# Optimization experiments

Hardware: AMD Instinct MI355X
Metric: run time of the kernel (lower is better)

## Reference

```python
import jax, jax.numpy as jnp
import numpy as np

N, C, D = 131072, 512, 3


def setup_inputs() -> dict:
    key = jax.random.key(0)
    kx, kmu = jax.random.split(key)
    X = jax.random.normal(kx, (N, D), dtype=jnp.float32)
    mu = jax.random.normal(kmu, (C, D), dtype=jnp.float32)
    w = jnp.zeros((C,), dtype=jnp.float32)
    # sigma as in __init__: r = sqrt(sum of per-dim unbiased variances of mu0)
    r = jnp.sqrt(jnp.var(mu, axis=0, ddof=1).sum())
    sigma = (0.1 * (r / C ** (1.0 / D))).astype(jnp.float32)
    return {"X": X, "mu": mu, "w": w, "sigma": sigma}


def reference(X, mu, w, sigma):
    # One EM step of a uniform-covariance GMM (EM_step_pytorch).
    n, d = X.shape
    # pairwise squared distances [N, C]
    D2_nc = ((X[:, None, :] - mu[None, :, :]) ** 2).sum(-1)
    # log-responsibilities (E-step), softmax over components
    lgamma_nc = jax.nn.log_softmax(w[None, :] - D2_nc / (2.0 * sigma ** 2), axis=1)
    gamma_nc = jnp.exp(lgamma_nc)
    # M-step: centroids (softmax over points, per component)
    mu_new = jax.nn.softmax(lgamma_nc, axis=0).T @ X  # [C, D]
    # M-step: component scores
    h_c = jax.nn.logsumexp(lgamma_nc, axis=0)  # [C]
    w_new = h_c - h_c.mean()
    # M-step: uniform std
    sigma_new = jnp.sqrt((gamma_nc * D2_nc).sum() / (d * n))
    # EM values: expected targets and free energy
    Y = gamma_nc @ mu_new  # [N, D]
    logpi_c = w_new - jax.nn.logsumexp(w_new)
    Cfe = (gamma_nc * (
        ((mu_new ** 2).sum(-1)[None, :] - (Y ** 2).sum(-1)[:, None]) / (2.0 * sigma_new ** 2)
        + d * jnp.log(sigma_new)
        - logpi_c[None, :]
        + lgamma_nc
    )).sum()
    return Y, Cfe
```

## Files before the change

kernel.cpp:

```cpp
#include <hip/hip_runtime.h>
#include <cfloat>
#include <cmath>

#define NPTS 131072
#define NC   512
#define NREP 4

#define PM4_OFF  0
#define PQ4_OFF  2048
#define ST4_OFF  4096
#define MISC_OFF 12288

__device__ __forceinline__ float waveSum(float v) {
#pragma unroll
  for (int off = 32; off > 0; off >>= 1) v += __shfl_down(v, off, 64);
  return v;
}
__device__ __forceinline__ float waveMax(float v) {
#pragma unroll
  for (int off = 32; off > 0; off >>= 1) v = fmaxf(v, __shfl_down(v, off, 64));
  return v;
}

__global__ __launch_bounds__(512) void k_prep(
    const float* __restrict__ mu, const float* __restrict__ w,
    const float* __restrict__ sigma, float4* __restrict__ pm,
    float* __restrict__ ST, float* __restrict__ misc) {
  const int t = threadIdx.x;
  const float sg = sigma[0];
  const float inv2s2 = 1.0f / (2.0f * sg * sg);
  const float m0 = mu[3 * t], m1 = mu[3 * t + 1], m2 = mu[3 * t + 2];
  pm[t] = make_float4(2.0f * inv2s2 * m0, 2.0f * inv2s2 * m1, 2.0f * inv2s2 * m2,
                      w[t] - (m0 * m0 + m1 * m1 + m2 * m2) * inv2s2);
#pragma unroll
  for (int r = 0; r < NREP * 4; ++r) ST[r * 512 + t] = 0.f;
  if (t < 8) misc[t] = 0.f;
}

__global__ __launch_bounds__(512, 8) void k_estep(
    const float* __restrict__ X, const float4* __restrict__ pm,
    float* __restrict__ ST, float* __restrict__ misc,
    float* __restrict__ out) {
  __shared__ float4 s_pt[128];
  __shared__ float2 s_ms[4][128];
  __shared__ float  s_red[8];
  __shared__ float  s_red2[8];

  const int t = threadIdx.x;
  const int p = t & 127;
  const int ch = __builtin_amdgcn_readfirstlane(t >> 7);
  const int n = blockIdx.x * 128 + p;
  const float x0 = X[3 * n], x1 = X[3 * n + 1], x2 = X[3 * n + 2];

  const float4* __restrict__ pmc = pm + ch * 128;
  float ma = -FLT_MAX, mb = -FLT_MAX, mc = -FLT_MAX, md = -FLT_MAX;
#pragma unroll 4
  for (int i = 0; i < 128; i += 4) {
    float4 a = pmc[i], b = pmc[i + 1], c = pmc[i + 2], d = pmc[i + 3];
    ma = fmaxf(ma, fmaf(a.x, x0, fmaf(a.y, x1, fmaf(a.z, x2, a.w))));
    mb = fmaxf(mb, fmaf(b.x, x0, fmaf(b.y, x1, fmaf(b.z, x2, b.w))));
    mc = fmaxf(mc, fmaf(c.x, x0, fmaf(c.y, x1, fmaf(c.z, x2, c.w))));
    md = fmaxf(md, fmaf(d.x, x0, fmaf(d.y, x1, fmaf(d.z, x2, d.w))));
  }
  const float m = fmaxf(fmaxf(ma, mb), fmaxf(mc, md));
  float sa = 0.f, sb = 0.f, sc = 0.f, sd = 0.f;
#pragma unroll 4
  for (int i = 0; i < 128; i += 4) {
    float4 a = pmc[i], b = pmc[i + 1], c = pmc[i + 2], d = pmc[i + 3];
    sa += __expf(fmaf(a.x, x0, fmaf(a.y, x1, fmaf(a.z, x2, a.w))) - m);
    sb += __expf(fmaf(b.x, x0, fmaf(b.y, x1, fmaf(b.z, x2, b.w))) - m);
    sc += __expf(fmaf(c.x, x0, fmaf(c.y, x1, fmaf(c.z, x2, c.w))) - m);
    sd += __expf(fmaf(d.x, x0, fmaf(d.y, x1, fmaf(d.z, x2, d.w))) - m);
  }
  s_ms[ch][p] = make_float2(m, (sa + sb) + (sc + sd));
  __syncthreads();

  if (t < 128) {
    float2 q0 = s_ms[0][t], q1 = s_ms[1][t], q2 = s_ms[2][t], q3 = s_ms[3][t];
    float M = fmaxf(fmaxf(q0.x, q1.x), fmaxf(q2.x, q3.x));
    float SS = q0.y * __expf(q0.x - M) + q1.y * __expf(q1.x - M) +
               q2.y * __expf(q2.x - M) + q3.y * __expf(q3.x - M);
    float z = M + __logf(SS);
    s_pt[t] = make_float4(x0, x1, x2, z);
    out[3 * n] = z;
  }
  __syncthreads();

  const float4 pc = pm[t];
  float Sg = 0.f, Tx = 0.f, Ty = 0.f, Tz = 0.f, La = 0.f;
#pragma unroll 4
  for (int i = 0; i < 128; ++i) {
    float4 pt = s_pt[i];
    float l = fmaf(pc.x, pt.x, fmaf(pc.y, pt.y, fmaf(pc.z, pt.z, pc.w)));
    float d = l - pt.w;
    float g = __expf(d);
    Sg += g;
    Tx = fmaf(g, pt.x, Tx);
    Ty = fmaf(g, pt.y, Ty);
    Tz = fmaf(g, pt.z, Tz);
    La = fmaf(g, d, La);
  }
  float* st = ST + (((blockIdx.x & (NREP - 1)) * 512 + t) << 2);
  atomicAdd(st + 0, Tx);
  atomicAdd(st + 1, Ty);
  atomicAdd(st + 2, Tz);
  atomicAdd(st + 3, Sg);

  float xx = (t < 128) ? (x0 * x0 + x1 * x1 + x2 * x2) : 0.f;
  float rx = waveSum(xx);
  float rl = waveSum(La);
  if ((t & 63) == 0) { s_red[t >> 6] = rx; s_red2[t >> 6] = rl; }
  __syncthreads();
  if (t == 0) {
    float vx = 0.f, vl = 0.f;
#pragma unroll
    for (int i = 0; i < 8; ++i) { vx += s_red[i]; vl += s_red2[i]; }
    atomicAdd(&misc[0], vx);
    atomicAdd(&misc[3], vl);
  }
}

__global__ __launch_bounds__(512) void k_mstep(
    const float* __restrict__ mu, const float4* __restrict__ ST4,
    float4* __restrict__ pq, float* __restrict__ misc,
    float* __restrict__ out) {
  __shared__ float s_red[8];
  __shared__ float s_red2[8];
  __shared__ float s_bc[4];
  const int t = threadIdx.x;

  float Tx = 0.f, Ty = 0.f, Tz = 0.f, S = 0.f;
#pragma unroll
  for (int r = 0; r < NREP; ++r) {
    float4 v = ST4[r * 512 + t];
    Tx += v.x; Ty += v.y; Tz += v.z; S += v.w;
  }
  const float Sc = fmaxf(S, 1e-30f);
  const float h = __logf(Sc);
  const float m0 = Tx / Sc, m1 = Ty / Sc, m2 = Tz / Sc;

  const float o0 = mu[3 * t], o1 = mu[3 * t + 1], o2 = mu[3 * t + 2];
  const float gdp = S * (o0 * o0 + o1 * o1 + o2 * o2)
                    - 2.0f * (o0 * Tx + o1 * Ty + o2 * Tz);

  float hm = waveMax(h);
  if ((t & 63) == 0) s_red[t >> 6] = hm;
  __syncthreads();
  if (t == 0) {
    float v = s_red[0];
    for (int i = 1; i < 8; ++i) v = fmaxf(v, s_red[i]);
    s_bc[0] = v;
  }
  __syncthreads();
  const float hM = s_bc[0];

  float es = waveSum(__expf(h - hM));
  float gs = waveSum(gdp);
  if ((t & 63) == 0) { s_red[t >> 6] = es; s_red2[t >> 6] = gs; }
  __syncthreads();
  if (t == 0) {
    float esum = 0.f, gsum = 0.f;
    for (int i = 0; i < 8; ++i) { esum += s_red[i]; gsum += s_red2[i]; }
    s_bc[1] = hM + __logf(esum);
    const float gd = fmaxf(misc[0] + gsum, 1e-20f);
    const float sn2 = gd * (1.0f / (3.0f * (float)NPTS));
    s_bc[2] = 1.0f / (2.0f * sn2);
    s_bc[3] = 1.5f * __logf(sn2);
  }
  __syncthreads();

  const float inv2s2n = s_bc[2];
  const float logpi = h - s_bc[1];
  const float A = (m0 * m0 + m1 * m1 + m2 * m2) * inv2s2n - logpi;
  pq[t] = make_float4(m0, m1, m2, A);

  float ca = waveSum(S * A);
  if ((t & 63) == 0) s_red[t >> 6] = ca;
  __syncthreads();
  if (t == 0) {
    float v = 0.f;
    for (int i = 0; i < 8; ++i) v += s_red[i];
    out[NPTS * 3] = v + misc[3] + (float)NPTS * s_bc[3];
    misc[1] = inv2s2n;
  }
}

__global__ __launch_bounds__(512, 8) void k_final(
    const float* __restrict__ X, const float4* __restrict__ pm,
    const float4* __restrict__ pq, const float* __restrict__ misc,
    float* __restrict__ out) {
  __shared__ float4 s_y[4][128];
  __shared__ float  s_red[8];

  const int t = threadIdx.x;
  const int p = t & 127;
  const int ch = __builtin_amdgcn_readfirstlane(t >> 7);
  const int n = blockIdx.x * 128 + p;
  const float x0 = X[3 * n], x1 = X[3 * n + 1], x2 = X[3 * n + 2];
  const float z = out[3 * n];
  const float inv2s2n = misc[1];

  const float4* __restrict__ pmc = pm + ch * 128;
  const float4* __restrict__ pqc = pq + ch * 128;
  float y0 = 0.f, y1 = 0.f, y2 = 0.f;
#pragma unroll 4
  for (int i = 0; i < 128; ++i) {
    float4 pp = pmc[i];
    float4 qq = pqc[i];
    float l = fmaf(pp.x, x0, fmaf(pp.y, x1, fmaf(pp.z, x2, pp.w))) - z;
    float g = __expf(l);
    y0 = fmaf(g, qq.x, y0);
    y1 = fmaf(g, qq.y, y1);
    y2 = fmaf(g, qq.z, y2);
  }
  s_y[ch][p] = make_float4(y0, y1, y2, 0.f);
  __syncthreads();

  float cfe = 0.f;
  if (t < 128) {
    float4 a0 = s_y[0][t], a1 = s_y[1][t], a2 = s_y[2][t], a3 = s_y[3][t];
    float Y0 = (a0.x + a1.x) + (a2.x + a3.x);
    float Y1 = (a0.y + a1.y) + (a2.y + a3.y);
    float Y2 = (a0.z + a1.z) + (a2.z + a3.z);
    cfe = -(Y0 * Y0 + Y1 * Y1 + Y2 * Y2) * inv2s2n;
    out[3 * n] = Y0;
    out[3 * n + 1] = Y1;
    out[3 * n + 2] = Y2;
  }
  float r = waveSum(cfe);
  if ((t & 63) == 0) s_red[t >> 6] = r;
  __syncthreads();
  if (t == 0) {
    float v = 0.f;
#pragma unroll
    for (int i = 0; i < 8; ++i) v += s_red[i];
    atomicAdd(&out[NPTS * 3], v);
  }
}

extern "C" void kernel_launch(void* const* d_in, const int* in_sizes, int n_in,
                              void* d_out, int out_size, void* d_ws, size_t ws_size,
                              hipStream_t stream) {
  const float* X = (const float*)d_in[0];
  const float* mu = (const float*)d_in[1];
  const float* w = (const float*)d_in[2];
  const float* sigma = (const float*)d_in[3];
  float* out = (float*)d_out;
  float* ws = (float*)d_ws;

  float4* pm = (float4*)(ws + PM4_OFF);
  float4* pq = (float4*)(ws + PQ4_OFF);
  float* ST = ws + ST4_OFF;
  float* misc = ws + MISC_OFF;

  k_prep<<<1, 512, 0, stream>>>(mu, w, sigma, pm, ST, misc);
  k_estep<<<NPTS / 128, 512, 0, stream>>>(X, pm, ST, misc, out);
  k_mstep<<<1, 512, 0, stream>>>(mu, (const float4*)ST, pq, misc, out);
  k_final<<<NPTS / 128, 512, 0, stream>>>(X, pm, pq, misc, out);
}
```

Measured before the change: 146.0 us.

## Use base-2 exponent domain, 64-point tiles with 8 chunks, and analytic entropy term

```diff
diff --git a/kernel.cpp b/kernel.cpp
--- a/kernel.cpp
+++ b/kernel.cpp
@@ -4,12 +4,17 @@
 
 #define NPTS 131072
 #define NC   512
-#define NREP 4
+#define NREP 8
+#define LOG2E 1.44269504088896340736f
+#define LN2   0.69314718055994530942f
+
+__device__ __forceinline__ float fexp2(float x) { return __builtin_amdgcn_exp2f(x); }
+__device__ __forceinline__ float flog2(float x) { return __builtin_amdgcn_logf(x); }
 
 #define PM4_OFF  0
 #define PQ4_OFF  2048
-#define ST4_OFF  4096
-#define MISC_OFF 12288
+#define ST_OFF   4096
+#define MISC_OFF (ST_OFF + NREP * NC * 4)
 
 __device__ __forceinline__ float waveSum(float v) {
 #pragma unroll
@@ -24,126 +29,134 @@
 
 __global__ __launch_bounds__(512) void k_prep(
     const float* __restrict__ mu, const float* __restrict__ w,
-    const float* __restrict__ sigma, float4* __restrict__ pm,
-    float* __restrict__ ST, float* __restrict__ misc) {
+    const float* __restrict__ sigma, float* __restrict__ ws) {
   const int t = threadIdx.x;
   const float sg = sigma[0];
-  const float inv2s2 = 1.0f / (2.0f * sg * sg);
+  const float k = LOG2E / (2.0f * sg * sg);
   const float m0 = mu[3 * t], m1 = mu[3 * t + 1], m2 = mu[3 * t + 2];
-  pm[t] = make_float4(2.0f * inv2s2 * m0, 2.0f * inv2s2 * m1, 2.0f * inv2s2 * m2,
-                      w[t] - (m0 * m0 + m1 * m1 + m2 * m2) * inv2s2);
-#pragma unroll
-  for (int r = 0; r < NREP * 4; ++r) ST[r * 512 + t] = 0.f;
-  if (t < 8) misc[t] = 0.f;
+  float4* pm = (float4*)(ws + PM4_OFF);
+  pm[t] = make_float4(2.0f * k * m0, 2.0f * k * m1, 2.0f * k * m2,
+                      LOG2E * w[t] - (m0 * m0 + m1 * m1 + m2 * m2) * k);
+  float* ST = ws + ST_OFF;
+#pragma unroll
+  for (int r = 0; r < NREP * 4; ++r) ST[r * NC + t] = 0.f;
+  if (t < 8) ws[MISC_OFF + t] = 0.f;
 }
 
 __global__ __launch_bounds__(512, 8) void k_estep(
-    const float* __restrict__ X, const float4* __restrict__ pm,
-    float* __restrict__ ST, float* __restrict__ misc,
+    const float* __restrict__ X, float* __restrict__ ws,
     float* __restrict__ out) {
-  __shared__ float4 s_pt[128];
-  __shared__ float2 s_ms[4][128];
-  __shared__ float  s_red[8];
-  __shared__ float  s_red2[8];
-
-  const int t = threadIdx.x;
-  const int p = t & 127;
-  const int ch = __builtin_amdgcn_readfirstlane(t >> 7);
-  const int n = blockIdx.x * 128 + p;
+  __shared__ float4 s_pt[64];
+  __shared__ float4 s_ms[8][64];
+
+  float* __restrict__ ST = ws + ST_OFF;
+  float* __restrict__ misc = ws + MISC_OFF;
+  const float4* __restrict__ pm = (const float4*)(ws + PM4_OFF);
+
+  const int t = threadIdx.x;
+  const int p = t & 63;
+  const int ch = __builtin_amdgcn_readfirstlane(t >> 6);
+  const int n = blockIdx.x * 64 + p;
   const float x0 = X[3 * n], x1 = X[3 * n + 1], x2 = X[3 * n + 2];
 
-  const float4* __restrict__ pmc = pm + ch * 128;
-  float ma = -FLT_MAX, mb = -FLT_MAX, mc = -FLT_MAX, md = -FLT_MAX;
-#pragma unroll 4
-  for (int i = 0; i < 128; i += 4) {
-    float4 a = pmc[i], b = pmc[i + 1], c = pmc[i + 2], d = pmc[i + 3];
-    ma = fmaxf(ma, fmaf(a.x, x0, fmaf(a.y, x1, fmaf(a.z, x2, a.w))));
-    mb = fmaxf(mb, fmaf(b.x, x0, fmaf(b.y, x1, fmaf(b.z, x2, b.w))));
-    mc = fmaxf(mc, fmaf(c.x, x0, fmaf(c.y, x1, fmaf(c.z, x2, c.w))));
-    md = fmaxf(md, fmaf(d.x, x0, fmaf(d.y, x1, fmaf(d.z, x2, d.w))));
-  }
-  const float m = fmaxf(fmaxf(ma, mb), fmaxf(mc, md));
-  float sa = 0.f, sb = 0.f, sc = 0.f, sd = 0.f;
-#pragma unroll 4
-  for (int i = 0; i < 128; i += 4) {
-    float4 a = pmc[i], b = pmc[i + 1], c = pmc[i + 2], d = pmc[i + 3];
-    sa += __expf(fmaf(a.x, x0, fmaf(a.y, x1, fmaf(a.z, x2, a.w))) - m);
-    sb += __expf(fmaf(b.x, x0, fmaf(b.y, x1, fmaf(b.z, x2, b.w))) - m);
-    sc += __expf(fmaf(c.x, x0, fmaf(c.y, x1, fmaf(c.z, x2, c.w))) - m);
-    sd += __expf(fmaf(d.x, x0, fmaf(d.y, x1, fmaf(d.z, x2, d.w))) - m);
-  }
-  s_ms[ch][p] = make_float2(m, (sa + sb) + (sc + sd));
-  __syncthreads();
-
-  if (t < 128) {
-    float2 q0 = s_ms[0][t], q1 = s_ms[1][t], q2 = s_ms[2][t], q3 = s_ms[3][t];
-    float M = fmaxf(fmaxf(q0.x, q1.x), fmaxf(q2.x, q3.x));
-    float SS = q0.y * __expf(q0.x - M) + q1.y * __expf(q1.x - M) +
-               q2.y * __expf(q2.x - M) + q3.y * __expf(q3.x - M);
-    float z = M + __logf(SS);
-    s_pt[t] = make_float4(x0, x1, x2, z);
-    out[3 * n] = z;
-  }
-  __syncthreads();
-
-  const float4 pc = pm[t];
-  float Sg = 0.f, Tx = 0.f, Ty = 0.f, Tz = 0.f, La = 0.f;
-#pragma unroll 4
-  for (int i = 0; i < 128; ++i) {
-    float4 pt = s_pt[i];
-    float l = fmaf(pc.x, pt.x, fmaf(pc.y, pt.y, fmaf(pc.z, pt.z, pc.w)));
-    float d = l - pt.w;
-    float g = __expf(d);
-    Sg += g;
-    Tx = fmaf(g, pt.x, Tx);
-    Ty = fmaf(g, pt.y, Ty);
-    Tz = fmaf(g, pt.z, Tz);
-    La = fmaf(g, d, La);
-  }
-  float* st = ST + (((blockIdx.x & (NREP - 1)) * 512 + t) << 2);
-  atomicAdd(st + 0, Tx);
-  atomicAdd(st + 1, Ty);
-  atomicAdd(st + 2, Tz);
-  atomicAdd(st + 3, Sg);
-
-  float xx = (t < 128) ? (x0 * x0 + x1 * x1 + x2 * x2) : 0.f;
-  float rx = waveSum(xx);
-  float rl = waveSum(La);
-  if ((t & 63) == 0) { s_red[t >> 6] = rx; s_red2[t >> 6] = rl; }
-  __syncthreads();
-  if (t == 0) {
-    float vx = 0.f, vl = 0.f;
-#pragma unroll
-    for (int i = 0; i < 8; ++i) { vx += s_red[i]; vl += s_red2[i]; }
-    atomicAdd(&misc[0], vx);
-    atomicAdd(&misc[3], vl);
+  const float4* __restrict__ pmc = pm + ch * 64;
+  {
+    float ma = -FLT_MAX, mb = -FLT_MAX, mc = -FLT_MAX, md = -FLT_MAX;
+#pragma unroll 4
+    for (int i = 0; i < 64; i += 4) {
+      float4 a = pmc[i], b = pmc[i + 1], c = pmc[i + 2], d = pmc[i + 3];
+      ma = fmaxf(ma, fmaf(a.x, x0, fmaf(a.y, x1, fmaf(a.z, x2, a.w))));
+      mb = fmaxf(mb, fmaf(b.x, x0, fmaf(b.y, x1, fmaf(b.z, x2, b.w))));
+      mc = fmaxf(mc, fmaf(c.x, x0, fmaf(c.y, x1, fmaf(c.z, x2, c.w))));
+      md = fmaxf(md, fmaf(d.x, x0, fmaf(d.y, x1, fmaf(d.z, x2, d.w))));
+    }
+    const float m = fmaxf(fmaxf(ma, mb), fmaxf(mc, md));
+    float sa = 0.f, sb = 0.f, wa = 0.f, wb = 0.f;
+#pragma unroll 4
+    for (int i = 0; i < 64; i += 2) {
+      float4 a = pmc[i], b = pmc[i + 1];
+      float da = fmaf(a.x, x0, fmaf(a.y, x1, fmaf(a.z, x2, a.w))) - m;
+      float db = fmaf(b.x, x0, fmaf(b.y, x1, fmaf(b.z, x2, b.w))) - m;
+      float ea = fexp2(da);
+      float eb = fexp2(db);
+      sa += ea; wa = fmaf(ea, da, wa);
+      sb += eb; wb = fmaf(eb, db, wb);
+    }
+    s_ms[ch][p] = make_float4(m, sa + sb, wa + wb, 0.f);
+  }
+  __syncthreads();
+
+  float glg = 0.f, xx = 0.f;
+  if (t < 64) {
+    float M = -FLT_MAX;
+    float4 q[8];
+#pragma unroll
+    for (int i = 0; i < 8; ++i) { q[i] = s_ms[i][t]; M = fmaxf(M, q[i].x); }
+    float SS = 0.f;
+    float e[8];
+#pragma unroll
+    for (int i = 0; i < 8; ++i) { e[i] = fexp2(q[i].x - M); SS += e[i] * q[i].y; }
+    const float z2 = M + flog2(SS);
+    float gnum = 0.f;
+#pragma unroll
+    for (int i = 0; i < 8; ++i) gnum += e[i] * fmaf(q[i].x - z2, q[i].y, q[i].z);
+    glg = gnum / SS;
+    xx = x0 * x0 + x1 * x1 + x2 * x2;
+    s_pt[t] = make_float4(x0, x1, x2, z2);
+    out[3 * n] = z2;
+  }
+  {
+    float rl = waveSum(glg);
+    float rx = waveSum(xx);
+    if (t == 0) { atomicAdd(&misc[0], rx); atomicAdd(&misc[3], rl); }
+  }
+  __syncthreads();
+
+  {
+    const float4 pc = pm[t];
+    float Sg = 0.f, Tx = 0.f, Ty = 0.f, Tz = 0.f;
+#pragma unroll 4
+    for (int i = 0; i < 64; ++i) {
+      float4 pt = s_pt[i];
+      float l = fmaf(pc.x, pt.x, fmaf(pc.y, pt.y, fmaf(pc.z, pt.z, pc.w)));
+      float g = fexp2(l - pt.w);
+      Sg += g;
+      Tx = fmaf(g, pt.x, Tx);
+      Ty = fmaf(g, pt.y, Ty);
+      Tz = fmaf(g, pt.z, Tz);
+    }
+    float* st = ST + (((blockIdx.x & (NREP - 1)) * NC + t) << 2);
+    atomicAdd(st + 0, Tx);
+    atomicAdd(st + 1, Ty);
+    atomicAdd(st + 2, Tz);
+    atomicAdd(st + 3, Sg);
   }
 }
 
 __global__ __launch_bounds__(512) void k_mstep(
-    const float* __restrict__ mu, const float4* __restrict__ ST4,
-    float4* __restrict__ pq, float* __restrict__ misc,
+    const float* __restrict__ mu, float* __restrict__ ws,
     float* __restrict__ out) {
   __shared__ float s_red[8];
   __shared__ float s_red2[8];
   __shared__ float s_bc[4];
   const int t = threadIdx.x;
+  const float4* __restrict__ ST4 = (const float4*)(ws + ST_OFF);
+  float* __restrict__ misc = ws + MISC_OFF;
 
   float Tx = 0.f, Ty = 0.f, Tz = 0.f, S = 0.f;
 #pragma unroll
   for (int r = 0; r < NREP; ++r) {
-    float4 v = ST4[r * 512 + t];
+    float4 v = ST4[r * NC + t];
     Tx += v.x; Ty += v.y; Tz += v.z; S += v.w;
   }
   const float Sc = fmaxf(S, 1e-30f);
-  const float h = __logf(Sc);
+  const float h2 = flog2(Sc);
   const float m0 = Tx / Sc, m1 = Ty / Sc, m2 = Tz / Sc;
-
   const float o0 = mu[3 * t], o1 = mu[3 * t + 1], o2 = mu[3 * t + 2];
   const float gdp = S * (o0 * o0 + o1 * o1 + o2 * o2)
                     - 2.0f * (o0 * Tx + o1 * Ty + o2 * Tz);
 
-  float hm = waveMax(h);
+  float hm = waveMax(h2);
   if ((t & 63) == 0) s_red[t >> 6] = hm;
   __syncthreads();
   if (t == 0) {
@@ -153,62 +166,63 @@
   }
   __syncthreads();
   const float hM = s_bc[0];
-
-  float es = waveSum(__expf(h - hM));
+  float es = waveSum(fexp2(h2 - hM));
   float gs = waveSum(gdp);
   if ((t & 63) == 0) { s_red[t >> 6] = es; s_red2[t >> 6] = gs; }
   __syncthreads();
   if (t == 0) {
     float esum = 0.f, gsum = 0.f;
     for (int i = 0; i < 8; ++i) { esum += s_red[i]; gsum += s_red2[i]; }
-    s_bc[1] = hM + __logf(esum);
+    s_bc[1] = hM + flog2(esum);
     const float gd = fmaxf(misc[0] + gsum, 1e-20f);
     const float sn2 = gd * (1.0f / (3.0f * (float)NPTS));
     s_bc[2] = 1.0f / (2.0f * sn2);
-    s_bc[3] = 1.5f * __logf(sn2);
+    s_bc[3] = LN2 * 1.5f * flog2(sn2);
   }
   __syncthreads();
 
   const float inv2s2n = s_bc[2];
-  const float logpi = h - s_bc[1];
+  const float logpi = LN2 * (h2 - s_bc[1]);
   const float A = (m0 * m0 + m1 * m1 + m2 * m2) * inv2s2n - logpi;
-  pq[t] = make_float4(m0, m1, m2, A);
-
-  float ca = waveSum(S * A);
-  if ((t & 63) == 0) s_red[t >> 6] = ca;
+  ((float4*)(ws + PQ4_OFF))[t] = make_float4(m0, m1, m2, A);
+
+  float rs = waveSum(S * A);
+  if ((t & 63) == 0) s_red[t >> 6] = rs;
   __syncthreads();
   if (t == 0) {
     float v = 0.f;
     for (int i = 0; i < 8; ++i) v += s_red[i];
-    out[NPTS * 3] = v + misc[3] + (float)NPTS * s_bc[3];
+    out[NPTS * 3] = v + LN2 * misc[3] + (float)NPTS * s_bc[3];
     misc[1] = inv2s2n;
   }
 }
 
 __global__ __launch_bounds__(512, 8) void k_final(
-    const float* __restrict__ X, const float4* __restrict__ pm,
-    const float4* __restrict__ pq, const float* __restrict__ misc,
+    const float* __restrict__ X, const float* __restrict__ ws,
     float* __restrict__ out) {
-  __shared__ float4 s_y[4][128];
-  __shared__ float  s_red[8];
-
-  const int t = threadIdx.x;
-  const int p = t & 127;
-  const int ch = __builtin_amdgcn_readfirstlane(t >> 7);
-  const int n = blockIdx.x * 128 + p;
+  __shared__ float4 s_y[8][64];
+
+  const float4* __restrict__ pm = (const float4*)(ws + PM4_OFF);
+  const float4* __restrict__ pq = (const float4*)(ws + PQ4_OFF);
+  const float* __restrict__ misc = ws + MISC_OFF;
+
+  const int t = threadIdx.x;
+  const int p = t & 63;
+  const int ch = __builtin_amdgcn_readfirstlane(t >> 6);
+  const int n = blockIdx.x * 64 + p;
   const float x0 = X[3 * n], x1 = X[3 * n + 1], x2 = X[3 * n + 2];
-  const float z = out[3 * n];
+  const float z2 = out[3 * n];
   const float inv2s2n = misc[1];
 
-  const float4* __restrict__ pmc = pm + ch * 128;
-  const float4* __restrict__ pqc = pq + ch * 128;
+  const float4* __restrict__ pmc = pm + ch * 64;
+  const float4* __restrict__ pqc = pq + ch * 64;
   float y0 = 0.f, y1 = 0.f, y2 = 0.f;
 #pragma unroll 4
-  for (int i = 0; i < 128; ++i) {
+  for (int i = 0; i < 64; ++i) {
     float4 pp = pmc[i];
     float4 qq = pqc[i];
-    float l = fmaf(pp.x, x0, fmaf(pp.y, x1, fmaf(pp.z, x2, pp.w))) - z;
-    float g = __expf(l);
+    float l = fmaf(pp.x, x0, fmaf(pp.y, x1, fmaf(pp.z, x2, pp.w))) - z2;
+    float g = fexp2(l);
     y0 = fmaf(g, qq.x, y0);
     y1 = fmaf(g, qq.y, y1);
     y2 = fmaf(g, qq.z, y2);
@@ -217,25 +231,20 @@
   __syncthreads();
 
   float cfe = 0.f;
-  if (t < 128) {
-    float4 a0 = s_y[0][t], a1 = s_y[1][t], a2 = s_y[2][t], a3 = s_y[3][t];
-    float Y0 = (a0.x + a1.x) + (a2.x + a3.x);
-    float Y1 = (a0.y + a1.y) + (a2.y + a3.y);
-    float Y2 = (a0.z + a1.z) + (a2.z + a3.z);
+  if (t < 64) {
+    float Y0 = 0.f, Y1 = 0.f, Y2 = 0.f;
+#pragma unroll
+    for (int i = 0; i < 8; ++i) {
+      float4 a = s_y[i][t];
+      Y0 += a.x; Y1 += a.y; Y2 += a.z;
+    }
     cfe = -(Y0 * Y0 + Y1 * Y1 + Y2 * Y2) * inv2s2n;
     out[3 * n] = Y0;
     out[3 * n + 1] = Y1;
     out[3 * n + 2] = Y2;
   }
   float r = waveSum(cfe);
-  if ((t & 63) == 0) s_red[t >> 6] = r;
-  __syncthreads();
-  if (t == 0) {
-    float v = 0.f;
-#pragma unroll
-    for (int i = 0; i < 8; ++i) v += s_red[i];
-    atomicAdd(&out[NPTS * 3], v);
-  }
+  if (t == 0) atomicAdd(&out[NPTS * 3], r);
 }
 
 extern "C" void kernel_launch(void* const* d_in, const int* in_sizes, int n_in,
@@ -248,13 +257,8 @@
   float* out = (float*)d_out;
   float* ws = (float*)d_ws;
 
-  float4* pm = (float4*)(ws + PM4_OFF);
-  float4* pq = (float4*)(ws + PQ4_OFF);
-  float* ST = ws + ST4_OFF;
-  float* misc = ws + MISC_OFF;
-
-  k_prep<<<1, 512, 0, stream>>>(mu, w, sigma, pm, ST, misc);
-  k_estep<<<NPTS / 128, 512, 0, stream>>>(X, pm, ST, misc, out);
-  k_mstep<<<1, 512, 0, stream>>>(mu, (const float4*)ST, pq, misc, out);
-  k_final<<<NPTS / 128, 512, 0, stream>>>(X, pm, pq, misc, out);
-}
+  k_prep<<<1, 512, 0, stream>>>(mu, w, sigma, ws);
+  k_estep<<<NPTS / 64, 512, 0, stream>>>(X, ws, out);
+  k_mstep<<<1, 512, 0, stream>>>(mu, ws, out);
+  k_final<<<NPTS / 64, 512, 0, stream>>>(X, ws, out);
+}
```

After: 192.7 us. 32.0% more time.
